# Performance work log

Measured on AMD Instinct MI355X. Metric: run time of the kernel, lower is better.

The kernel has to match this reference:

```python
import jax, jax.numpy as jnp
import numpy as np
import math

B, D, H, DK = 24, 64, 8, 8
N, M, CN = 256, 64, 16
VW, VC, CE, WE = 30000, 128, 200, 300

FREQS = jnp.asarray(np.array([10000.0 ** (-i / D) if i % 2 == 0 else -(10000.0 ** (-(i - 1) / D)) for i in range(D)], dtype=np.float32)[:, None])
PHASES = jnp.asarray(np.array([0.0 if i % 2 == 0 else math.pi / 2 for i in range(D)], dtype=np.float32)[:, None])

def _norm(x, eps=1e-6):
    mu = x.mean(-1, keepdims=True)
    var = ((x - mu) ** 2).sum(-1, keepdims=True) / (x.shape[-1] - 1)  # torch std is unbiased
    return (x - mu) / (jnp.sqrt(var) + eps)

def _pos_enc(x):
    pos = jnp.arange(x.shape[-1], dtype=x.dtype)[None, :]
    return jnp.sin(jnp.sin(pos * FREQS + PHASES)) + x  # double sin kept faithful to source

def _conv1d(x, w, groups=1, pad=0, b=None):
    y = jax.lax.conv_general_dilated(x, w, (1,), [(pad, pad)], dimension_numbers=('NCH', 'OIH', 'NCH'), feature_group_count=groups)
    return y if b is None else y + b[None, :, None]

def _dwsep1d(x, dw, pw, db=None, pb=None):
    y = _conv1d(x, dw, groups=x.shape[1], pad=dw.shape[-1] // 2, b=db)
    return _conv1d(y, pw, b=pb)

def _conv2d(x, w, groups=1, pad=0, b=None):
    y = jax.lax.conv_general_dilated(x, w, (1, 1), [(pad, pad), (pad, pad)], dimension_numbers=('NCHW', 'OIHW', 'NCHW'), feature_group_count=groups)
    return y if b is None else y + b[None, :, None, None]

def _highway(x, lw, lb, gw, gb):
    x = x.transpose(0, 2, 1)  # [B,L,D]
    for i in range(lw.shape[0]):
        g = jax.nn.sigmoid(jnp.einsum('bld,od->blo', x, gw[i]) + gb[i])
        nl = jax.nn.relu(jnp.einsum('bld,od->blo', x, lw[i]) + lb[i])
        x = g * nl + (1.0 - g) * x
    return x.transpose(0, 2, 1)

def _embed(ch, wd, e2dw, e2db, e2pw, e2pb, e1dw, e1db, e1pw, e1pb, hlw, hlb, hgw, hgb):
    ch = ch.transpose(0, 3, 1, 2)  # [B,CE,L,CN]
    ch = _conv2d(ch, e2dw, groups=CE, pad=2, b=e2db)
    ch = _conv2d(ch, e2pw, b=e2pb)
    ch = jax.nn.relu(ch).max(axis=3)  # [B,D,L]
    wd = wd.transpose(0, 2, 1)  # [B,WE,L]
    emb = jnp.concatenate([ch, wd], axis=1)
    emb = _dwsep1d(emb, e1dw, e1pw, e1db, e1pb)
    return _highway(emb, hlw, hlb, hgw, hgb)

def _self_att(x, wq, wk, wv, wo):
    Qh = jnp.einsum('hbkd,bdl->hbkl', wq, x)
    Kh = jnp.einsum('hbkd,bdl->hbkl', wk, x)
    Vh = jnp.einsum('hbkd,bdl->hbkl', wv, x)
    scores = jnp.einsum('hbkl,hbkm->hblm', Qh, Kh) / math.sqrt(DK)
    att = jax.nn.softmax(scores, axis=2)  # torch softmax dim=1 over [B,l,m]
    head = jnp.einsum('hbvl,hblm->hbvm', Vh, att)
    head = head.transpose(1, 0, 2, 3).reshape(B, H * DK, x.shape[-1])
    return jnp.einsum('bod,bdl->bol', wo, head)

def _enc_block(x, dw, pw, wq, wk, wv, wo, W):
    out = _pos_enc(x)
    res = out
    for i in range(dw.shape[0]):
        out = jax.nn.relu(_dwsep1d(_norm(out), dw[i], pw[i]))
        out = res + out
        res = out  # dropout is a no-op in this deterministic reference
    out = res + _self_att(_norm(out), wq, wk, wv, wo)
    res = out
    out = jax.nn.relu(jnp.einsum('bod,bdl->bol', W, _norm(out)))
    return res + out

def _cq_att(C, Q, W):
    # S[b,i,j] = W . [Q[:,j]; C[:,i]; Q[:,j]*C[:,i]] -- vectorized trilinear similarity
    wq, wc, wm = W[:, 0, :D], W[:, 0, D:2 * D], W[:, 0, 2 * D:]
    S = (jnp.einsum('bd,bdn->bn', wc, C)[:, :, None]
         + jnp.einsum('bd,bdm->bm', wq, Q)[:, None, :]
         + jnp.einsum('bdn,bdm->bnm', C * wm[:, :, None], Q))
    S1 = jax.nn.softmax(S, axis=2)
    S2 = jax.nn.softmax(S, axis=1)
    A = jnp.einsum('bdm,bnm->bdn', Q, S1)
    X = jnp.einsum('bnm,bkm->bnk', S1, S2)  # S1 @ S2^T
    Bm = jnp.einsum('bdn,bkn->bdk', C, X)   # C @ X^T
    return jnp.concatenate([C, A, C * A, C * Bm], axis=1)

def _pointer(M0, M1, M2, w0, w1):
    Y0 = jnp.einsum('bd,bdn->bn', w0[:, 0], jnp.concatenate([M0, M1], axis=1))
    Y1 = jnp.einsum('bd,bdn->bn', w1[:, 0], jnp.concatenate([M0, M2], axis=1))
    return jax.nn.softmax(Y0, axis=1), jax.nn.softmax(Y1, axis=1)  # exp(log_softmax)

def _qanet(flt, Cwid, Ccid, Qwid, Qcid):
    (word_table, char_table,
     e2dw, e2db, e2pw, e2pb, e1dw, e1db, e1pw, e1pb,
     hlw, hlb, hgw, hgb,
     ce_dw, ce_pw, ce_wq, ce_wk, ce_wv, ce_wo, ce_w,
     qe_dw, qe_pw, qe_wq, qe_wk, qe_wv, qe_wo, qe_w,
     m0_dw, m0_pw, m0_wq, m0_wk, m0_wv, m0_wo, m0_w,
     m1_dw, m1_pw, m1_wq, m1_wk, m1_wv, m1_wo, m1_w,
     m2_dw, m2_pw, m2_wq, m2_wk, m2_wv, m2_wo, m2_w,
     cq_w, rs_dw, rs_pw, p_w0, p_w1) = flt
    emb_p = (e2dw, e2db, e2pw, e2pb, e1dw, e1db, e1pw, e1pb, hlw, hlb, hgw, hgb)
    C = _embed(char_table[Ccid], word_table[Cwid], *emb_p)
    Q = _embed(char_table[Qcid], word_table[Qwid], *emb_p)
    C = _enc_block(C, ce_dw, ce_pw, ce_wq, ce_wk, ce_wv, ce_wo, ce_w)
    Q = _enc_block(Q, qe_dw, qe_pw, qe_wq, qe_wk, qe_wv, qe_wo, qe_w)
    X = _cq_att(C, Q, cq_w)
    X = _dwsep1d(X, rs_dw, rs_pw)
    M0 = X
    for _ in range(7):
        M0 = _enc_block(M0, m0_dw, m0_pw, m0_wq, m0_wk, m0_wv, m0_wo, m0_w)
    M1 = M0
    for _ in range(7):
        M1 = _enc_block(M1, m1_dw, m1_pw, m1_wq, m1_wk, m1_wv, m1_wo, m1_w)
    M2 = M1
    for _ in range(7):
        M2 = _enc_block(M2, m2_dw, m2_pw, m2_wq, m2_wk, m2_wv, m2_wo, m2_w)
    return _pointer(M0, M1, M2, p_w0, p_w1)

def setup_inputs() -> dict:
    key = jax.random.key(0)
    ks = iter(jax.random.split(key, 80))
    rn = lambda shape, s=0.1: jax.random.normal(next(ks), shape, jnp.float32) * s
    inp = {}
    inp['word_table'] = rn((VW, WE), 1.0)
    inp['char_table'] = rn((VC, CE), 1.0)
    inp['e2dw'] = rn((CE, 1, 5, 5)); inp['e2db'] = jnp.zeros((CE,), jnp.float32)
    inp['e2pw'] = rn((D, CE, 1, 1)); inp['e2pb'] = jnp.zeros((D,), jnp.float32)
    inp['e1dw'] = rn((WE + D, 1, 5)); inp['e1db'] = jnp.zeros((WE + D,), jnp.float32)
    inp['e1pw'] = rn((D, WE + D, 1)); inp['e1pb'] = jnp.zeros((D,), jnp.float32)
    inp['hlw'] = rn((2, D, D)); inp['hlb'] = jnp.zeros((2, D), jnp.float32)
    inp['hgw'] = rn((2, D, D)); inp['hgb'] = jnp.zeros((2, D), jnp.float32)
    for p, (cnum, k_) in [('ce', (4, 7)), ('qe', (4, 7)), ('m0', (2, 5)), ('m1', (2, 5)), ('m2', (2, 5))]:
        inp[p + '_dw'] = rn((cnum, D, 1, k_))
        inp[p + '_pw'] = rn((cnum, D, D, 1))
        inp[p + '_wq'] = rn((H, B, DK, D))
        inp[p + '_wk'] = rn((H, B, DK, D))
        inp[p + '_wv'] = rn((H, B, DK, D))
        inp[p + '_wo'] = rn((B, D, D))
        inp[p + '_w'] = rn((B, D, D))
    inp['cq_w'] = rn((B, 1, 3 * D))
    inp['rs_dw'] = rn((4 * D, 1, 5))
    inp['rs_pw'] = rn((D, 4 * D, 1))
    inp['p_w0'] = rn((B, 1, 2 * D))
    inp['p_w1'] = rn((B, 1, 2 * D))
    inp['Cwid'] = jax.random.randint(next(ks), (B, N), 0, VW)
    inp['Ccid'] = jax.random.randint(next(ks), (B, N, CN), 0, VC)
    inp['Qwid'] = jax.random.randint(next(ks), (B, M), 0, VW)
    inp['Qcid'] = jax.random.randint(next(ks), (B, M, CN), 0, VC)
    return inp

def reference(word_table, char_table, e2dw, e2db, e2pw, e2pb, e1dw, e1db, e1pw, e1pb, hlw, hlb, hgw, hgb, ce_dw, ce_pw, ce_wq, ce_wk, ce_wv, ce_wo, ce_w, qe_dw, qe_pw, qe_wq, qe_wk, qe_wv, qe_wo, qe_w, m0_dw, m0_pw, m0_wq, m0_wk, m0_wv, m0_wo, m0_w, m1_dw, m1_pw, m1_wq, m1_wk, m1_wv, m1_wo, m1_w, m2_dw, m2_pw, m2_wq, m2_wk, m2_wv, m2_wo, m2_w, cq_w, rs_dw, rs_pw, p_w0, p_w1, Cwid, Ccid, Qwid, Qcid):
    flt = (word_table, char_table, e2dw, e2db, e2pw, e2pb, e1dw, e1db, e1pw, e1pb, hlw, hlb, hgw, hgb, ce_dw, ce_pw, ce_wq, ce_wk, ce_wv, ce_wo, ce_w, qe_dw, qe_pw, qe_wq, qe_wk, qe_wv, qe_wo, qe_w, m0_dw, m0_pw, m0_wq, m0_wk, m0_wv, m0_wo, m0_w, m1_dw, m1_pw, m1_wq, m1_wk, m1_wv, m1_wo, m1_w, m2_dw, m2_pw, m2_wq, m2_wk, m2_wv, m2_wo, m2_w, cq_w, rs_dw, rs_pw, p_w0, p_w1)
    p0, p1 = _qanet(flt, Cwid, Ccid, Qwid, Qcid)
    return p0, p1
```

## Files before the change

kernel.cpp:

```cpp
#include <hip/hip_runtime.h>
#include <math.h>

constexpr int B = 24, HH = 8;
constexpr int NN = 256, MQ = 64;
constexpr int EC = 364;

#define PI_2 1.5707963267948966f

__device__ __forceinline__ void combine_stats(const float* __restrict__ parts,
                                              int row, int NT, float Lf,
                                              float& mu, float& inv) {
  float s = 0.f, q = 0.f;
  for (int t = 0; t < NT; ++t) {
    s += parts[((size_t)row * 4 + t) * 2];
    q += parts[((size_t)row * 4 + t) * 2 + 1];
  }
  mu = s / Lf;
  float var = (q - s * mu) / (Lf - 1.f);
  if (var < 0.f) var = 0.f;
  inv = 1.f / (sqrtf(var) + 1e-6f);
}

__global__ void k_prep(float* __restrict__ tab,
                       const float* __restrict__ e2pw, const float* __restrict__ e1pw,
                       const float* __restrict__ hlw, const float* __restrict__ hgw,
                       const float* __restrict__ e2dw,
                       float* __restrict__ pwT, float* __restrict__ e1pwT,
                       float* __restrict__ hlwT, float* __restrict__ hgwT,
                       float* __restrict__ dwT) {
  int blk = blockIdx.x;
  if (blk < 64) {
    int d = blk, l = threadIdx.x;
    float fr = ((d & 1) == 0) ? powf(10000.f, -(float)d / 64.f)
                              : -powf(10000.f, -(float)(d - 1) / 64.f);
    float ph = (d & 1) ? PI_2 : 0.f;
    tab[d * 256 + l] = sinf(sinf((float)l * fr + ph));
    return;
  }
  int i = (blk - 64) * 256 + threadIdx.x;
  if (i < 12800) {
    int ce = i >> 6, o = i & 63;
    pwT[i] = e2pw[o * 200 + ce];
    return;
  }
  i -= 12800;
  if (i < 23296) {
    int c = i >> 6, o = i & 63;
    e1pwT[i] = e1pw[o * EC + c];
    return;
  }
  i -= 23296;
  if (i < 8192) {
    int layer = i >> 12, rem = i & 4095;
    int d = rem >> 6, o = rem & 63;
    hlwT[i] = hlw[layer * 4096 + o * 64 + d];
    return;
  }
  i -= 8192;
  if (i < 8192) {
    int layer = i >> 12, rem = i & 4095;
    int d = rem >> 6, o = rem & 63;
    hgwT[i] = hgw[layer * 4096 + o * 64 + d];
    return;
  }
  i -= 8192;
  if (i < 5000) {
    int t = i / 200, ce = i % 200;
    dwT[i] = e2dw[ce * 25 + t];
  }
}

__global__ void k_posadd_stats(float* __restrict__ XC, float* __restrict__ XQ,
                               const float* __restrict__ tab,
                               float* __restrict__ partsC, float* __restrict__ partsQ) {
  int which = blockIdx.y;
  float* X = which ? XQ : XC;
  float* parts = which ? partsQ : partsC;
  int L = which ? 64 : 256;
  int row = blockIdx.x * 4 + (threadIdx.x >> 6);
  int lane = threadIdx.x & 63;
  int d = row & 63;
  float* xr = X + (size_t)row * L;
  int NT = L >> 6;
  for (int t = 0; t < NT; ++t) {
    int l = t * 64 + lane;
    float v = xr[l] + tab[d * 256 + l];
    xr[l] = v;
    float s = v, q = v * v;
#pragma unroll
    for (int o = 32; o > 0; o >>= 1) { s += __shfl_xor(s, o); q += __shfl_xor(q, o); }
    if (lane == 0) {
      parts[((size_t)row * 4 + t) * 2] = s;
      parts[((size_t)row * 4 + t) * 2 + 1] = q;
    }
  }
}

template<int K>
__global__ __launch_bounds__(1024) void k_fconv(
    const float* __restrict__ XiC, float* __restrict__ XoC,
    const float* __restrict__ XiQ, float* __restrict__ XoQ,
    const float* __restrict__ dwC, const float* __restrict__ pwC,
    const float* __restrict__ dwQ, const float* __restrict__ pwQ,
    const float* __restrict__ pinC, float* __restrict__ poutC,
    const float* __restrict__ pinQ, float* __restrict__ poutQ) {
  constexpr int H = K / 2, SW = 64 + 2 * H;
  __shared__ float smu[64], sinv[64];
  __shared__ float sN[64 * SW];
  __shared__ float sD[64 * 65];
  __shared__ __align__(16) float sWt[4096];
  int b = blockIdx.x, t = blockIdx.y;
  const float *Xin, *dw, *pw, *pin; float *Xout, *pout; int L, tile;
  if (t < 4) { Xin = XiC; Xout = XoC; dw = dwC; pw = pwC; pin = pinC; pout = poutC; L = 256; tile = t; }
  else       { Xin = XiQ; Xout = XoQ; dw = dwQ; pw = pwQ; pin = pinQ; pout = poutQ; L = 64;  tile = 0; }
  int lt = tile * 64;
  int tid = threadIdx.x;
  int NT = L >> 6;
  if (tid < 64) combine_stats(pin, b * 64 + tid, NT, (float)L, smu[tid], sinv[tid]);
  for (int i = tid; i < 1024; i += 1024)
    ((float4*)sWt)[i] = ((const float4*)pw)[i];
  const float* Xb = Xin + (size_t)b * 64 * L;
  int l = tid & 63, og = tid >> 6;
  float rres[4];
#pragma unroll
  for (int j = 0; j < 4; ++j)
    rres[j] = Xb[(size_t)(og * 4 + j) * L + lt + l];
  __syncthreads();
  for (int i = tid; i < 64 * SW; i += 1024) {
    int c = i / SW, jj = i % SW;
    int gl = lt + jj - H;
    sN[i] = (gl >= 0 && gl < L) ? (Xb[(size_t)c * L + gl] - smu[c]) * sinv[c] : 0.f;
  }
  __syncthreads();
  for (int i = tid; i < 4096; i += 1024) {
    int c = i >> 6, ll = i & 63;
    float acc = 0.f;
#pragma unroll
    for (int k = 0; k < K; ++k) acc += sN[c * SW + ll + k] * dw[c * K + k];
    sD[c * 65 + ll] = acc;
  }
  __syncthreads();
  float acc[4];
#pragma unroll
  for (int j = 0; j < 4; ++j) acc[j] = 0.f;
  for (int c = 0; c < 64; ++c) {
    float av = sD[c * 65 + l];
#pragma unroll
    for (int j = 0; j < 4; ++j) acc[j] += sWt[(og * 4 + j) * 64 + c] * av;
  }
  __syncthreads();
  float* Ob = Xout + (size_t)b * 64 * L;
#pragma unroll
  for (int j = 0; j < 4; ++j) {
    int o = og * 4 + j;
    float v = rres[j] + fmaxf(acc[j], 0.f);
    Ob[(size_t)o * L + lt + l] = v;
    sD[o * 65 + l] = v;
  }
  __syncthreads();
  if (tid < 64) {
    int o = tid;
    float s = 0.f, q = 0.f;
    for (int l2 = 0; l2 < 64; ++l2) { float v = sD[o * 65 + l2]; s += v; q += v * v; }
    pout[((size_t)(b * 64 + o) * 4 + tile) * 2] = s;
    pout[((size_t)(b * 64 + o) * 4 + tile) * 2 + 1] = q;
  }
}

template<bool NORM, bool RELU, bool STATS, bool ADDTAB, bool DUAL>
__global__ __launch_bounds__(1024) void k_matmul2(
    const float* __restrict__ AC, const float* __restrict__ WC,
    const float* __restrict__ resC, float* __restrict__ outC2,
    const float* __restrict__ pinC, float* __restrict__ poutC,
    const float* __restrict__ AQ, const float* __restrict__ WQ,
    const float* __restrict__ resQ, float* __restrict__ outQ2,
    const float* __restrict__ pinQ, float* __restrict__ poutQ,
    float* __restrict__ outNextC, const float* __restrict__ tab) {
  __shared__ float sA[64 * 65];
  __shared__ __align__(16) float sW[4096];
  __shared__ float smu[64], sinv[64];
  int b = blockIdx.x, t = blockIdx.y;
  const float *A, *W, *res, *pin; float *outp, *pout; int L, tile;
  if (t < 4) { A = AC; W = WC; res = resC; outp = outC2; pin = pinC; pout = poutC; L = 256; tile = t; }
  else       { A = AQ; W = WQ; res = resQ; outp = outQ2; pin = pinQ; pout = poutQ; L = 64;  tile = 0; }
  int lt = tile * 64;
  int tid = threadIdx.x;
  int NT = L >> 6;
  if (NORM && tid < 64) combine_stats(pin, b * 64 + tid, NT, (float)L, smu[tid], sinv[tid]);
  const float* Wb = W + (size_t)b * 4096;
  for (int i = tid; i < 1024; i += 1024)
    ((float4*)sW)[i] = ((const float4*)Wb)[i];
  int l = tid & 63, og = tid >> 6;
  float rres[4], rtab[4];
#pragma unroll
  for (int j = 0; j < 4; ++j) {
    int o = og * 4 + j;
    rres[j] = res[((size_t)b * 64 + o) * L + lt + l];
    if (ADDTAB || DUAL) rtab[j] = tab[o * 256 + lt + l];
  }
  if (NORM) __syncthreads();
  const float* Ab = A + (size_t)b * 64 * L;
  for (int i = tid; i < 1024; i += 1024) {
    int c = i >> 4, lq = (i & 15) * 4;
    float4 v = *(const float4*)(Ab + (size_t)c * L + lt + lq);
    if (NORM) {
      float mu = smu[c], iv = sinv[c];
      v.x = (v.x - mu) * iv; v.y = (v.y - mu) * iv;
      v.z = (v.z - mu) * iv; v.w = (v.w - mu) * iv;
    }
    sA[c * 65 + lq] = v.x; sA[c * 65 + lq + 1] = v.y;
    sA[c * 65 + lq + 2] = v.z; sA[c * 65 + lq + 3] = v.w;
  }
  __syncthreads();
  float acc[4];
#pragma unroll
  for (int j = 0; j < 4; ++j) acc[j] = 0.f;
  for (int c = 0; c < 64; ++c) {
    float av = sA[c * 65 + l];
#pragma unroll
    for (int j = 0; j < 4; ++j) acc[j] += sW[(og * 4 + j) * 64 + c] * av;
  }
  if (STATS) __syncthreads();
#pragma unroll
  for (int j = 0; j < 4; ++j) {
    int o = og * 4 + j;
    float v = acc[j];
    if (RELU) v = fmaxf(v, 0.f);
    v += rres[j];
    if (DUAL) {
      float vn = v + rtab[j];
      outp[((size_t)b * 64 + o) * L + lt + l] = v;
      outNextC[((size_t)b * 64 + o) * L + lt + l] = vn;
      if (STATS) sA[o * 65 + l] = vn;
    } else {
      if (ADDTAB) v += rtab[j];
      outp[((size_t)b * 64 + o) * L + lt + l] = v;
      if (STATS) sA[o * 65 + l] = v;
    }
  }
  if (STATS) {
    __syncthreads();
    if (tid < 64) {
      int o = tid;
      float s = 0.f, q = 0.f;
      for (int l2 = 0; l2 < 64; ++l2) { float v = sA[o * 65 + l2]; s += v; q += v * v; }
      pout[((size_t)(b * 64 + o) * 4 + tile) * 2] = s;
      pout[((size_t)(b * 64 + o) * 4 + tile) * 2 + 1] = q;
    }
  }
}

__global__ __launch_bounds__(256) void k_resize(
    const float* __restrict__ Xcat, const float* __restrict__ dw,
    const float* __restrict__ pw, const float* __restrict__ tab,
    float* __restrict__ out, float* __restrict__ parts) {
  __shared__ float sA[64 * 65];
  int b = blockIdx.x, lt = blockIdx.y * 64;
  int l = threadIdx.x & 63, og = threadIdx.x >> 6;
  float acc[16];
#pragma unroll
  for (int j = 0; j < 16; ++j) acc[j] = 0.f;
  for (int c0 = 0; c0 < 256; c0 += 64) {
    __syncthreads();
    for (int i = threadIdx.x; i < 4096; i += 256) {
      int c = (i >> 6) + c0, ll = (i & 63) + lt;
      const float* xr = Xcat + ((size_t)b * 256 + c) * 256;
      float a = 0.f;
#pragma unroll
      for (int k = 0; k < 5; ++k) {
        int p = ll + k - 2;
        if (p >= 0 && p < 256) a += xr[p] * dw[c * 5 + k];
      }
      sA[(i >> 6) * 65 + (i & 63)] = a;
    }
    __syncthreads();
    for (int c = 0; c < 64; ++c) {
      float av = sA[c * 65 + l];
#pragma unroll
      for (int j = 0; j < 16; ++j)
        acc[j] += pw[(size_t)(og * 16 + j) * 256 + c0 + c] * av;
    }
  }
  __syncthreads();
#pragma unroll
  for (int j = 0; j < 16; ++j) {
    int o = og * 16 + j;
    float v = acc[j] + tab[o * 256 + lt + l];
    out[((size_t)b * 64 + o) * 256 + lt + l] = v;
    sA[o * 65 + l] = v;
  }
  __syncthreads();
  if (threadIdx.x < 64) {
    int o = threadIdx.x;
    float s = 0.f, q = 0.f;
    for (int l2 = 0; l2 < 64; ++l2) { float v = sA[o * 65 + l2]; s += v; q += v * v; }
    parts[((size_t)(b * 64 + o) * 4 + blockIdx.y) * 2] = s;
    parts[((size_t)(b * 64 + o) * 4 + blockIdx.y) * 2 + 1] = q;
  }
}

__global__ __launch_bounds__(1024) void k_att(
    const float* __restrict__ XC, const float* __restrict__ partsC,
    const float* __restrict__ wqC, const float* __restrict__ wkC,
    const float* __restrict__ wvC, float* __restrict__ hcC,
    const float* __restrict__ XQ, const float* __restrict__ partsQ,
    const float* __restrict__ wqQ, const float* __restrict__ wkQ,
    const float* __restrict__ wvQ, float* __restrict__ hcQ) {
  int h = blockIdx.x, b2 = blockIdx.y;
  const float *X, *parts, *wq, *wk, *wv; float* hc; int L, b;
  if (b2 < B) { X = XC; parts = partsC; wq = wqC; wk = wkC; wv = wvC; hc = hcC; L = 256; b = b2; }
  else        { X = XQ; parts = partsQ; wq = wqQ; wk = wkQ; wv = wvQ; hc = hcQ; L = 64;  b = b2 - B; }
  __shared__ float smu[64], sinv[64];
  __shared__ float sX[64 * 65];
  __shared__ float sQ[2048], sK8[2048], sV[2048];
  __shared__ float swq[512], swk[512], swv[512];
  __shared__ float pmx[1024], psum[1024];
  int tid = threadIdx.x;
  int NT = L >> 6;
  if (tid < 64) combine_stats(parts, b * 64 + tid, NT, (float)L, smu[tid], sinv[tid]);
  size_t woff = (size_t)(h * B + b) * 512;
  if (tid < 512) {
    swq[tid] = wq[woff + tid];
    swk[tid] = wk[woff + tid];
    swv[tid] = wv[woff + tid];
  }
  __syncthreads();
  const float* Xb = X + (size_t)b * 64 * L;
  for (int lt = 0; lt < L; lt += 64) {
    for (int i = tid; i < 4096; i += 1024) {
      int d = i >> 6, l = i & 63;
      sX[d * 65 + l] = (Xb[(size_t)d * L + lt + l] - smu[d]) * sinv[d];
    }
    __syncthreads();
    if (tid < 512) {
      int k = tid >> 6, l = tid & 63;
      float aq = 0.f, ak = 0.f, av = 0.f;
      for (int d = 0; d < 64; ++d) {
        float x = sX[d * 65 + l];
        aq += swq[k * 64 + d] * x;
        ak += swk[k * 64 + d] * x;
        av += swv[k * 64 + d] * x;
      }
      sQ[k * L + lt + l] = aq; sK8[k * L + lt + l] = ak; sV[k * L + lt + l] = av;
    }
    __syncthreads();
  }
  const float scale = 0.35355339059327373f;
  int m = tid & 255, qt = tid >> 8;
  int L4 = L >> 2;
  float mx = -1e30f, sum = 0.f, acc[8];
#pragma unroll
  for (int v = 0; v < 8; ++v) acc[v] = 0.f;
  if (m < L) {
    float kc[8];
#pragma unroll
    for (int k = 0; k < 8; ++k) kc[k] = sK8[k * L + m];
    int l0 = qt * L4, l1 = l0 + L4;
    for (int l = l0; l < l1; ++l) {
      float s = 0.f;
#pragma unroll
      for (int k = 0; k < 8; ++k) s += sQ[k * L + l] * kc[k];
      s *= scale;
      if (s <= mx) {
        float p = __expf(s - mx);
        sum += p;
#pragma unroll
        for (int v = 0; v < 8; ++v) acc[v] += p * sV[v * L + l];
      } else {
        float corr = __expf(mx - s);
        sum = sum * corr + 1.f;
#pragma unroll
        for (int v = 0; v < 8; ++v) acc[v] = acc[v] * corr + sV[v * L + l];
// ... 349 lines not shown
  out[sel * 6144 + b * 256 + n] = e / s;
}

extern "C" void kernel_launch(void* const* d_in, const int* in_sizes, int n_in,
                              void* d_out, int out_size, void* d_ws, size_t ws_size,
                              hipStream_t stream) {
  const float* word_table = (const float*)d_in[0];
  const float* char_table = (const float*)d_in[1];
  const float* e2dw = (const float*)d_in[2];
  const float* e2db = (const float*)d_in[3];
  const float* e2pw = (const float*)d_in[4];
  const float* e2pb = (const float*)d_in[5];
  const float* e1dw = (const float*)d_in[6];
  const float* e1db = (const float*)d_in[7];
  const float* e1pw = (const float*)d_in[8];
  const float* e1pb = (const float*)d_in[9];
  const float* hlw = (const float*)d_in[10];
  const float* hlb = (const float*)d_in[11];
  const float* hgw = (const float*)d_in[12];
  const float* hgb = (const float*)d_in[13];
  const float *enc_dw[5], *enc_pw[5], *enc_wq[5], *enc_wk[5], *enc_wv[5], *enc_wo[5], *enc_w[5];
  for (int p = 0; p < 5; ++p) {
    enc_dw[p] = (const float*)d_in[14 + 7 * p + 0];
    enc_pw[p] = (const float*)d_in[14 + 7 * p + 1];
    enc_wq[p] = (const float*)d_in[14 + 7 * p + 2];
    enc_wk[p] = (const float*)d_in[14 + 7 * p + 3];
    enc_wv[p] = (const float*)d_in[14 + 7 * p + 4];
    enc_wo[p] = (const float*)d_in[14 + 7 * p + 5];
    enc_w[p]  = (const float*)d_in[14 + 7 * p + 6];
  }
  const float* cq_w  = (const float*)d_in[49];
  const float* rs_dw = (const float*)d_in[50];
  const float* rs_pw = (const float*)d_in[51];
  const float* p_w0  = (const float*)d_in[52];
  const float* p_w1  = (const float*)d_in[53];
  const int* Cwid = (const int*)d_in[54];
  const int* Ccid = (const int*)d_in[55];
  const int* Qwid = (const int*)d_in[56];
  const int* Qcid = (const int*)d_in[57];
  float* out = (float*)d_out;

  float* ws = (float*)d_ws;
  float* postab = ws;
  float* U    = ws + 16384;
  float* Xcat = ws + 409600;
  float* CX   = ws + 1982464;
  float* Sb   = ws + 2375680;
  float* QX   = ws + 2768896;
  float* CS2  = ws + 2867200;
  float* rmax = ws + 2965504;
  float* rsum = ws + 2971648;
  float* cmax = ws + 2977792;
  float* csum = ws + 2979328;
  float* P0   = ws + 2980864;
  float* P1   = ws + 2993152;
  float* pwT  = ws + 3005440;
  float* e1pwT= ws + 3018240;
  float* hlwT = ws + 3041536;
  float* hgwT = ws + 3049728;
  float* dwT  = ws + 3057920;
  float* P0Q  = ws + 3062920;
  float* P1Q  = ws + 3075208;
  float* UQ   = ws + 3087496;
  float* M0 = CX; float* M1 = Sb; float* M2 = Xcat;
  float* E1C = Xcat;
  float* E1Q = Xcat + 393216;
  (void)out_size; (void)in_sizes; (void)n_in; (void)ws_size;

  auto run_enc = [&](float* X, float* Xnext, int p) {
    for (int rep = 0; rep < 7; ++rep) {
      float* pin = P0; float* pout = P1;
      float* Xi = X; float* Xo = U;
      for (int i = 0; i < 2; ++i) {
        hipLaunchKernelGGL((k_fconv<5>), dim3(B, 4), dim3(1024), 0, stream,
                           (const float*)Xi, Xo, (const float*)nullptr, (float*)nullptr,
                           enc_dw[p] + i * 64 * 5, enc_pw[p] + (size_t)i * 4096,
                           (const float*)nullptr, (const float*)nullptr,
                           pin, pout, (const float*)nullptr, (float*)nullptr);
        { float* t = pin; pin = pout; pout = t; }
        { float* t = Xi; Xi = Xo; Xo = t; }
      }
      k_att<<<dim3(HH, B), 1024, 0, stream>>>(X, pin, enc_wq[p], enc_wk[p], enc_wv[p], U,
                                              (const float*)nullptr, (const float*)nullptr,
                                              (const float*)nullptr, (const float*)nullptr,
                                              (const float*)nullptr, (float*)nullptr);
      hipLaunchKernelGGL((k_matmul2<false, false, true, false, false>), dim3(B, 4), dim3(1024), 0, stream,
                         (const float*)U, enc_wo[p], (const float*)X, X, (const float*)nullptr, pout,
                         (const float*)nullptr, (const float*)nullptr, (const float*)nullptr,
                         (float*)nullptr, (const float*)nullptr, (float*)nullptr,
                         (float*)nullptr, (const float*)nullptr);
      if (rep < 6)
        hipLaunchKernelGGL((k_matmul2<true, true, true, true, false>), dim3(B, 4), dim3(1024), 0, stream,
                           (const float*)X, enc_w[p], (const float*)X, X, pout, P0,
                           (const float*)nullptr, (const float*)nullptr, (const float*)nullptr,
                           (float*)nullptr, (const float*)nullptr, (float*)nullptr,
                           (float*)nullptr, (const float*)postab);
      else if (Xnext)
        hipLaunchKernelGGL((k_matmul2<true, true, true, false, true>), dim3(B, 4), dim3(1024), 0, stream,
                           (const float*)X, enc_w[p], (const float*)X, X, pout, P0,
                           (const float*)nullptr, (const float*)nullptr, (const float*)nullptr,
                           (float*)nullptr, (const float*)nullptr, (float*)nullptr,
                           Xnext, (const float*)postab);
      else
        hipLaunchKernelGGL((k_matmul2<true, true, false, false, false>), dim3(B, 4), dim3(1024), 0, stream,
                           (const float*)X, enc_w[p], (const float*)X, X, pout, (float*)nullptr,
                           (const float*)nullptr, (const float*)nullptr, (const float*)nullptr,
                           (float*)nullptr, (const float*)nullptr, (float*)nullptr,
                           (float*)nullptr, (const float*)nullptr);
    }
  };

  k_prep<<<289, 256, 0, stream>>>(postab, e2pw, e1pw, hlw, hgw, e2dw,
                                  pwT, e1pwT, hlwT, hgwT, dwT);
  k_charembed<<<dim3(NN + MQ, B), 256, 0, stream>>>(Ccid, Qcid, char_table, dwT, e2db, pwT, e2pb, E1C, E1Q);
  k_embhw<<<dim3(NN + MQ, B), 64, 0, stream>>>(E1C, E1Q, Cwid, Qwid, word_table, e1dw, e1db,
                                               e1pwT, e1pb, hlwT, hlb, hgwT, hgb, CX, QX);
  {
    k_posadd_stats<<<dim3(384, 2), 256, 0, stream>>>(CX, QX, postab, P0, P0Q);
    float *pinC = P0, *poutC = P1, *pinQ = P0Q, *poutQ = P1Q;
    float *XiC = CX, *XoC = U, *XiQ = QX, *XoQ = UQ;
    for (int i = 0; i < 4; ++i) {
      hipLaunchKernelGGL((k_fconv<7>), dim3(B, 5), dim3(1024), 0, stream,
                         (const float*)XiC, XoC, (const float*)XiQ, XoQ,
                         enc_dw[0] + i * 64 * 7, enc_pw[0] + (size_t)i * 4096,
                         enc_dw[1] + i * 64 * 7, enc_pw[1] + (size_t)i * 4096,
                         pinC, poutC, pinQ, poutQ);
      { float* t = pinC; pinC = poutC; poutC = t; }
      { float* t = pinQ; pinQ = poutQ; poutQ = t; }
      { float* t = XiC; XiC = XoC; XoC = t; }
      { float* t = XiQ; XiQ = XoQ; XoQ = t; }
    }
    k_att<<<dim3(HH, 2 * B), 1024, 0, stream>>>(CX, pinC, enc_wq[0], enc_wk[0], enc_wv[0], U,
                                                QX, pinQ, enc_wq[1], enc_wk[1], enc_wv[1], UQ);
    hipLaunchKernelGGL((k_matmul2<false, false, true, false, false>), dim3(B, 5), dim3(1024), 0, stream,
                       (const float*)U, enc_wo[0], (const float*)CX, CX, (const float*)nullptr, poutC,
                       (const float*)UQ, enc_wo[1], (const float*)QX, QX, (const float*)nullptr, poutQ,
                       (float*)nullptr, (const float*)nullptr);
    hipLaunchKernelGGL((k_matmul2<true, true, false, false, false>), dim3(B, 5), dim3(1024), 0, stream,
                       (const float*)CX, enc_w[0], (const float*)CX, CX, poutC, (float*)nullptr,
                       (const float*)QX, enc_w[1], (const float*)QX, QX, poutQ, (float*)nullptr,
                       (float*)nullptr, (const float*)nullptr);
  }
  k_cqS<<<dim3(B, 4), 256, 0, stream>>>(CX, QX, cq_w, Sb, rmax, rsum);
  k_cqcol<<<B, 64, 0, stream>>>(Sb, cmax, csum);
  k_cqA_CS2<<<dim3(B, 5), 256, 0, stream>>>(CX, QX, Sb, rmax, rsum, cmax, csum, Xcat, CS2);
  k_cqBm<<<dim3(B, 4), 256, 0, stream>>>(CX, CS2, Sb, rmax, rsum, Xcat);
  k_resize<<<dim3(B, 4), 256, 0, stream>>>(Xcat, rs_dw, rs_pw, postab, M0, P0);
  run_enc(M0, M1, 2);
  run_enc(M1, M2, 3);
  run_enc(M2, nullptr, 4);
  k_pointer2<<<dim3(B, 2), 256, 0, stream>>>(M0, M1, M2, p_w0, p_w1, out);
}
```

Baseline: 1.999 ms.

## Fuse encoder conv pairs and wo/FFN into per-batch whole-sequence kernels

```diff
diff --git a/kernel.cpp b/kernel.cpp
--- a/kernel.cpp
+++ b/kernel.cpp
@@ -6,19 +6,29 @@
 constexpr int EC = 364;
 
 #define PI_2 1.5707963267948966f
-
-__device__ __forceinline__ void combine_stats(const float* __restrict__ parts,
-                                              int row, int NT, float Lf,
-                                              float& mu, float& inv) {
+#define CONV_LDS (36992 * 4)
+#define SMALL_LDS (18560 * 4)
+
+__device__ __forceinline__ void block_stats(const float* __restrict__ sX,
+                                            float* __restrict__ scratch,
+                                            float* __restrict__ smu,
+                                            float* __restrict__ sinv,
+                                            int L, int tid) {
+  int row = tid >> 4, sub = tid & 15;
   float s = 0.f, q = 0.f;
-  for (int t = 0; t < NT; ++t) {
-    s += parts[((size_t)row * 4 + t) * 2];
-    q += parts[((size_t)row * 4 + t) * 2 + 1];
-  }
-  mu = s / Lf;
-  float var = (q - s * mu) / (Lf - 1.f);
-  if (var < 0.f) var = 0.f;
-  inv = 1.f / (sqrtf(var) + 1e-6f);
+  for (int l2 = sub; l2 < L; l2 += 16) { float v = sX[row * L + l2]; s += v; q += v * v; }
+  scratch[row * 16 + sub] = s;
+  scratch[1024 + row * 16 + sub] = q;
+  __syncthreads();
+  if (tid < 64) {
+    float ss = 0.f, qq = 0.f;
+    for (int k = 0; k < 16; ++k) { ss += scratch[tid * 16 + k]; qq += scratch[1024 + tid * 16 + k]; }
+    float mu = ss / (float)L;
+    float var = (qq - ss * mu) / ((float)L - 1.f);
+    if (var < 0.f) var = 0.f;
+    smu[tid] = mu; sinv[tid] = 1.f / (sqrtf(var) + 1e-6f);
+  }
+  __syncthreads();
 }
 
 __global__ void k_prep(float* __restrict__ tab,
@@ -38,17 +48,9 @@
     return;
   }
   int i = (blk - 64) * 256 + threadIdx.x;
-  if (i < 12800) {
-    int ce = i >> 6, o = i & 63;
-    pwT[i] = e2pw[o * 200 + ce];
-    return;
-  }
+  if (i < 12800) { int ce = i >> 6, o = i & 63; pwT[i] = e2pw[o * 200 + ce]; return; }
   i -= 12800;
-  if (i < 23296) {
-    int c = i >> 6, o = i & 63;
-    e1pwT[i] = e1pw[o * EC + c];
-    return;
-  }
+  if (i < 23296) { int c = i >> 6, o = i & 63; e1pwT[i] = e1pw[o * EC + c]; return; }
   i -= 23296;
   if (i < 8192) {
     int layer = i >> 12, rem = i & 4095;
@@ -64,206 +66,194 @@
     return;
   }
   i -= 8192;
-  if (i < 5000) {
-    int t = i / 200, ce = i % 200;
-    dwT[i] = e2dw[ce * 25 + t];
-  }
-}
-
-__global__ void k_posadd_stats(float* __restrict__ XC, float* __restrict__ XQ,
-                               const float* __restrict__ tab,
-                               float* __restrict__ partsC, float* __restrict__ partsQ) {
-  int which = blockIdx.y;
-  float* X = which ? XQ : XC;
-  float* parts = which ? partsQ : partsC;
-  int L = which ? 64 : 256;
-  int row = blockIdx.x * 4 + (threadIdx.x >> 6);
-  int lane = threadIdx.x & 63;
-  int d = row & 63;
-  float* xr = X + (size_t)row * L;
-  int NT = L >> 6;
-  for (int t = 0; t < NT; ++t) {
-    int l = t * 64 + lane;
-    float v = xr[l] + tab[d * 256 + l];
-    xr[l] = v;
-    float s = v, q = v * v;
-#pragma unroll
-    for (int o = 32; o > 0; o >>= 1) { s += __shfl_xor(s, o); q += __shfl_xor(q, o); }
-    if (lane == 0) {
-      parts[((size_t)row * 4 + t) * 2] = s;
-      parts[((size_t)row * 4 + t) * 2 + 1] = q;
-    }
-  }
+  if (i < 5000) { int t = i / 200, ce = i % 200; dwT[i] = e2dw[ce * 25 + t]; }
+}
+
+__global__ __launch_bounds__(1024) void k_posadd(float* __restrict__ XC, float* __restrict__ XQ,
+                                                 const float* __restrict__ tab,
+                                                 float* __restrict__ SMc, float* __restrict__ SIc,
+                                                 float* __restrict__ SMq, float* __restrict__ SIq) {
+  extern __shared__ float sm[];
+  float* sX = sm; float* scratch = sm + 16384; float* smu = sm + 18432; float* sinv = sm + 18496;
+  int b = blockIdx.x, side = blockIdx.y;
+  float* X = side ? XQ : XC;
+  int L = side ? 64 : 256;
+  float* SM = side ? SMq : SMc;
+  float* SI = side ? SIq : SIc;
+  int tid = threadIdx.x;
+  float* Xb = X + (size_t)b * 64 * L;
+  for (int i = tid; i < 64 * L; i += 1024) {
+    int d = i / L, l = i % L;
+    float v = Xb[i] + tab[d * 256 + l];
+    Xb[i] = v; sX[i] = v;
+  }
+  __syncthreads();
+  block_stats(sX, scratch, smu, sinv, L, tid);
+  if (tid < 64) { SM[b * 64 + tid] = smu[tid]; SI[b * 64 + tid] = sinv[tid]; }
+}
+
+template<int K, int L>
+__device__ void conv2_impl(float* __restrict__ sm, float* __restrict__ X,
+                           const float* __restrict__ dw, const float* __restrict__ pw,
+                           float* __restrict__ SM, float* __restrict__ SI, int b, int nconv) {
+  constexpr int PER = (64 * L) / 1024;
+  float* sX = sm; float* sD = sm + 16384; float* sW = sm + 32768;
+  float* smu = sm + 36864; float* sinv = sm + 36928;
+  int tid = threadIdx.x;
+  int l = tid % L, og = tid / L;
+  float* Xb = X + (size_t)b * 64 * L;
+  for (int i = tid; i < 64 * L; i += 1024) sX[i] = Xb[i];
+  if (tid < 64) { smu[tid] = SM[b * 64 + tid]; sinv[tid] = SI[b * 64 + tid]; }
+  __syncthreads();
+  for (int cv = 0; cv < nconv; ++cv) {
+    {
+      const float* pwc = pw + cv * 4096;
+      for (int i = tid; i < 1024; i += 1024)
+        ((float4*)sW)[i] = ((const float4*)pwc)[i];
+    }
+    for (int i = tid; i < 64 * L; i += 1024) {
+      int c = i / L, ll = i % L;
+      float mu = smu[c], iv = sinv[c];
+      float acc = 0.f;
+#pragma unroll
+      for (int k = 0; k < K; ++k) {
+        int p = ll + k - K / 2;
+        float x = (p >= 0 && p < L) ? (sX[c * L + p] - mu) * iv : 0.f;
+        acc += x * dw[cv * 64 * K + c * K + k];
+      }
+      sD[i] = acc;
+    }
+    __syncthreads();
+    float acc[PER];
+#pragma unroll
+    for (int j = 0; j < PER; ++j) acc[j] = 0.f;
+    for (int c = 0; c < 64; ++c) {
+      float av = sD[c * L + l];
+#pragma unroll
+      for (int j = 0; j < PER; ++j) acc[j] += sW[(og * PER + j) * 64 + c] * av;
+    }
+#pragma unroll
+    for (int j = 0; j < PER; ++j) {
+      int o = og * PER + j;
+      sX[o * L + l] = sX[o * L + l] + fmaxf(acc[j], 0.f);
+    }
+    __syncthreads();
+    block_stats(sX, sD, smu, sinv, L, tid);
+  }
+  for (int i = tid; i < 64 * L; i += 1024) Xb[i] = sX[i];
+  if (tid < 64) { SM[b * 64 + tid] = smu[tid]; SI[b * 64 + tid] = sinv[tid]; }
 }
 
 template<int K>
-__global__ __launch_bounds__(1024) void k_fconv(
-    const float* __restrict__ XiC, float* __restrict__ XoC,
-    const float* __restrict__ XiQ, float* __restrict__ XoQ,
-    const float* __restrict__ dwC, const float* __restrict__ pwC,
-    const float* __restrict__ dwQ, const float* __restrict__ pwQ,
-    const float* __restrict__ pinC, float* __restrict__ poutC,
-    const float* __restrict__ pinQ, float* __restrict__ poutQ) {
-  constexpr int H = K / 2, SW = 64 + 2 * H;
-  __shared__ float smu[64], sinv[64];
-  __shared__ float sN[64 * SW];
-  __shared__ float sD[64 * 65];
-  __shared__ __align__(16) float sWt[4096];
-  int b = blockIdx.x, t = blockIdx.y;
-  const float *Xin, *dw, *pw, *pin; float *Xout, *pout; int L, tile;
-  if (t < 4) { Xin = XiC; Xout = XoC; dw = dwC; pw = pwC; pin = pinC; pout = poutC; L = 256; tile = t; }
-  else       { Xin = XiQ; Xout = XoQ; dw = dwQ; pw = pwQ; pin = pinQ; pout = poutQ; L = 64;  tile = 0; }
-  int lt = tile * 64;
+__global__ __launch_bounds__(1024) void k_conv2(
+    float* XC, float* XQ,
+    const float* dwC, const float* pwC, const float* dwQ, const float* pwQ,
+    float* SMc, float* SIc, float* SMq, float* SIq, int nconv) {
+  extern __shared__ float sm[];
+  int b = blockIdx.x;
+  if (blockIdx.y == 0) conv2_impl<K, 256>(sm, XC, dwC, pwC, SMc, SIc, b, nconv);
+  else                 conv2_impl<K, 64>(sm, XQ, dwQ, pwQ, SMq, SIq, b, nconv);
+}
+
+template<int L>
+__device__ void woff_impl(float* __restrict__ sm, const float* __restrict__ U,
+                          float* __restrict__ X, const float* __restrict__ wo,
+                          const float* __restrict__ w, float* __restrict__ SM,
+                          float* __restrict__ SI, float* __restrict__ Xnext,
+                          const float* __restrict__ tab, int b, int mode) {
+  constexpr int PER = (64 * L) / 1024;
+  float* sX = sm; float* sD = sm + 16384; float* sW = sm + 32768;
+  float* smu = sm + 36864; float* sinv = sm + 36928;
   int tid = threadIdx.x;
-  int NT = L >> 6;
-  if (tid < 64) combine_stats(pin, b * 64 + tid, NT, (float)L, smu[tid], sinv[tid]);
-  for (int i = tid; i < 1024; i += 1024)
-    ((float4*)sWt)[i] = ((const float4*)pw)[i];
-  const float* Xb = Xin + (size_t)b * 64 * L;
-  int l = tid & 63, og = tid >> 6;
-  float rres[4];
-#pragma unroll
-  for (int j = 0; j < 4; ++j)
-    rres[j] = Xb[(size_t)(og * 4 + j) * L + lt + l];
-  __syncthreads();
-  for (int i = tid; i < 64 * SW; i += 1024) {
-    int c = i / SW, jj = i % SW;
-    int gl = lt + jj - H;
-    sN[i] = (gl >= 0 && gl < L) ? (Xb[(size_t)c * L + gl] - smu[c]) * sinv[c] : 0.f;
-  }
-  __syncthreads();
-  for (int i = tid; i < 4096; i += 1024) {
-    int c = i >> 6, ll = i & 63;
-    float acc = 0.f;
-#pragma unroll
-    for (int k = 0; k < K; ++k) acc += sN[c * SW + ll + k] * dw[c * K + k];
-    sD[c * 65 + ll] = acc;
-  }
-  __syncthreads();
-  float acc[4];
-#pragma unroll
-  for (int j = 0; j < 4; ++j) acc[j] = 0.f;
+  int l = tid % L, og = tid / L;
+  const float* Ub = U + (size_t)b * 64 * L;
+  float* Xb = X + (size_t)b * 64 * L;
+  for (int i = tid; i < 64 * L; i += 1024) { sX[i] = Ub[i]; sD[i] = Xb[i]; }
+  {
+    const float* Wb = wo + (size_t)b * 4096;
+    for (int i = tid; i < 1024; i += 1024)
+      ((float4*)sW)[i] = ((const float4*)Wb)[i];
+  }
+  __syncthreads();
+  float acc[PER];
+#pragma unroll
+  for (int j = 0; j < PER; ++j) acc[j] = 0.f;
   for (int c = 0; c < 64; ++c) {
-    float av = sD[c * 65 + l];
-#pragma unroll
-    for (int j = 0; j < 4; ++j) acc[j] += sWt[(og * 4 + j) * 64 + c] * av;
-  }
-  __syncthreads();
-  float* Ob = Xout + (size_t)b * 64 * L;
-#pragma unroll
-  for (int j = 0; j < 4; ++j) {
-    int o = og * 4 + j;
-    float v = rres[j] + fmaxf(acc[j], 0.f);
-    Ob[(size_t)o * L + lt + l] = v;
-    sD[o * 65 + l] = v;
-  }
-  __syncthreads();
-  if (tid < 64) {
-    int o = tid;
-    float s = 0.f, q = 0.f;
-    for (int l2 = 0; l2 < 64; ++l2) { float v = sD[o * 65 + l2]; s += v; q += v * v; }
-    pout[((size_t)(b * 64 + o) * 4 + tile) * 2] = s;
-    pout[((size_t)(b * 64 + o) * 4 + tile) * 2 + 1] = q;
-  }
-}
-
-template<bool NORM, bool RELU, bool STATS, bool ADDTAB, bool DUAL>
-__global__ __launch_bounds__(1024) void k_matmul2(
-    const float* __restrict__ AC, const float* __restrict__ WC,
-    const float* __restrict__ resC, float* __restrict__ outC2,
-    const float* __restrict__ pinC, float* __restrict__ poutC,
-    const float* __restrict__ AQ, const float* __restrict__ WQ,
-    const float* __restrict__ resQ, float* __restrict__ outQ2,
-    const float* __restrict__ pinQ, float* __restrict__ poutQ,
-    float* __restrict__ outNextC, const float* __restrict__ tab) {
-  __shared__ float sA[64 * 65];
-  __shared__ __align__(16) float sW[4096];
-  __shared__ float smu[64], sinv[64];
-  int b = blockIdx.x, t = blockIdx.y;
-  const float *A, *W, *res, *pin; float *outp, *pout; int L, tile;
-  if (t < 4) { A = AC; W = WC; res = resC; outp = outC2; pin = pinC; pout = poutC; L = 256; tile = t; }
-  else       { A = AQ; W = WQ; res = resQ; outp = outQ2; pin = pinQ; pout = poutQ; L = 64;  tile = 0; }
-  int lt = tile * 64;
-  int tid = threadIdx.x;
-  int NT = L >> 6;
-  if (NORM && tid < 64) combine_stats(pin, b * 64 + tid, NT, (float)L, smu[tid], sinv[tid]);
-  const float* Wb = W + (size_t)b * 4096;
-  for (int i = tid; i < 1024; i += 1024)
-    ((float4*)sW)[i] = ((const float4*)Wb)[i];
-  int l = tid & 63, og = tid >> 6;
-  float rres[4], rtab[4];
-#pragma unroll
-  for (int j = 0; j < 4; ++j) {
-    int o = og * 4 + j;
-    rres[j] = res[((size_t)b * 64 + o) * L + lt + l];
-    if (ADDTAB || DUAL) rtab[j] = tab[o * 256 + lt + l];
-  }
-  if (NORM) __syncthreads();
-  const float* Ab = A + (size_t)b * 64 * L;
-  for (int i = tid; i < 1024; i += 1024) {
-    int c = i >> 4, lq = (i & 15) * 4;
-    float4 v = *(const float4*)(Ab + (size_t)c * L + lt + lq);
-    if (NORM) {
-      float mu = smu[c], iv = sinv[c];
-      v.x = (v.x - mu) * iv; v.y = (v.y - mu) * iv;
-      v.z = (v.z - mu) * iv; v.w = (v.w - mu) * iv;
-    }
-    sA[c * 65 + lq] = v.x; sA[c * 65 + lq + 1] = v.y;
-    sA[c * 65 + lq + 2] = v.z; sA[c * 65 + lq + 3] = v.w;
-  }
-  __syncthreads();
-  float acc[4];
-#pragma unroll
-  for (int j = 0; j < 4; ++j) acc[j] = 0.f;
+    float av = sX[c * L + l];
+#pragma unroll
+    for (int j = 0; j < PER; ++j) acc[j] += sW[(og * PER + j) * 64 + c] * av;
+  }
+  __syncthreads();
+#pragma unroll
+  for (int j = 0; j < PER; ++j) {
+    int o = og * PER + j;
+    sX[o * L + l] = sD[o * L + l] + acc[j];
+  }
+  __syncthreads();
+  block_stats(sX, sD, smu, sinv, L, tid);
+  {
+    const float* Wb = w + (size_t)b * 4096;
+    for (int i = tid; i < 1024; i += 1024)
+      ((float4*)sW)[i] = ((const float4*)Wb)[i];
+  }
+  __syncthreads();
+#pragma unroll
+  for (int j = 0; j < PER; ++j) acc[j] = 0.f;
   for (int c = 0; c < 64; ++c) {
-    float av = sA[c * 65 + l];
-#pragma unroll
-    for (int j = 0; j < 4; ++j) acc[j] += sW[(og * 4 + j) * 64 + c] * av;
-  }
-  if (STATS) __syncthreads();
-#pragma unroll
-  for (int j = 0; j < 4; ++j) {
-    int o = og * 4 + j;
-    float v = acc[j];
-    if (RELU) v = fmaxf(v, 0.f);
-    v += rres[j];
-    if (DUAL) {
-      float vn = v + rtab[j];
-      outp[((size_t)b * 64 + o) * L + lt + l] = v;
-      outNextC[((size_t)b * 64 + o) * L + lt + l] = vn;
-      if (STATS) sA[o * 65 + l] = vn;
+    float av = (sX[c * L + l] - smu[c]) * sinv[c];
+#pragma unroll
+    for (int j = 0; j < PER; ++j) acc[j] += sW[(og * PER + j) * 64 + c] * av;
+  }
+  __syncthreads();
+#pragma unroll
+  for (int j = 0; j < PER; ++j) {
+    int o = og * PER + j;
+    float v = sX[o * L + l] + fmaxf(acc[j], 0.f);
+    if (mode == 0) {
+      float vn = v + tab[o * 256 + l];
+      Xb[o * L + l] = vn; sX[o * L + l] = vn;
+    } else if (mode == 1) {
+      float vn = v + tab[o * 256 + l];
+      Xb[o * L + l] = v;
+      Xnext[(size_t)b * 64 * L + o * L + l] = vn;
+      sX[o * L + l] = vn;
     } else {
-      if (ADDTAB) v += rtab[j];
-      outp[((size_t)b * 64 + o) * L + lt + l] = v;
-      if (STATS) sA[o * 65 + l] = v;
-    }
-  }
-  if (STATS) {
-    __syncthreads();
-    if (tid < 64) {
-      int o = tid;
-      float s = 0.f, q = 0.f;
-      for (int l2 = 0; l2 < 64; ++l2) { float v = sA[o * 65 + l2]; s += v; q += v * v; }
-      pout[((size_t)(b * 64 + o) * 4 + tile) * 2] = s;
-      pout[((size_t)(b * 64 + o) * 4 + tile) * 2 + 1] = q;
-    }
-  }
-}
-
-__global__ __launch_bounds__(256) void k_resize(
+      Xb[o * L + l] = v;
+    }
+  }
+  if (mode < 2) {
+    __syncthreads();
+    block_stats(sX, sD, smu, sinv, L, tid);
+    if (tid < 64) { SM[b * 64 + tid] = smu[tid]; SI[b * 64 + tid] = sinv[tid]; }
+  }
+}
+
+__global__ __launch_bounds__(1024) void k_woff(
+    const float* UC, const float* UQ, float* XC, float* XQ,
+    const float* woC, const float* woQ, const float* wC, const float* wQ,
+    float* SMc, float* SIc, float* SMq, float* SIq,
+    float* Xnext, const float* tab, int mode) {
+  extern __shared__ float sm[];
+  int b = blockIdx.x;
+  if (blockIdx.y == 0) woff_impl<256>(sm, UC, XC, woC, wC, SMc, SIc, Xnext, tab, b, mode);
+  else                 woff_impl<64>(sm, UQ, XQ, woQ, wQ, SMq, SIq, nullptr, tab, b, mode);
+}
+
+__global__ __launch_bounds__(1024) void k_resize(
     const float* __restrict__ Xcat, const float* __restrict__ dw,
     const float* __restrict__ pw, const float* __restrict__ tab,
-    float* __restrict__ out, float* __restrict__ parts) {
-  __shared__ float sA[64 * 65];
-  int b = blockIdx.x, lt = blockIdx.y * 64;
-  int l = threadIdx.x & 63, og = threadIdx.x >> 6;
+    float* __restrict__ out, float* __restrict__ SM, float* __restrict__ SI) {
+  extern __shared__ float sm[];
+  float* sA = sm; float* scratch = sm + 16384; float* smu = sm + 18432; float* sinv = sm + 18496;
+  int b = blockIdx.x, tid = threadIdx.x;
+  int l = tid & 255, og = tid >> 8;
   float acc[16];
 #pragma unroll
   for (int j = 0; j < 16; ++j) acc[j] = 0.f;
   for (int c0 = 0; c0 < 256; c0 += 64) {
     __syncthreads();
-    for (int i = threadIdx.x; i < 4096; i += 256) {
-      int c = (i >> 6) + c0, ll = (i & 63) + lt;
+    for (int i = tid; i < 16384; i += 1024) {
+      int c = (i >> 8) + c0, ll = i & 255;
       const float* xr = Xcat + ((size_t)b * 256 + c) * 256;
       float a = 0.f;
 #pragma unroll
@@ -271,11 +261,11 @@
         int p = ll + k - 2;
         if (p >= 0 && p < 256) a += xr[p] * dw[c * 5 + k];
       }
-      sA[(i >> 6) * 65 + (i & 63)] = a;
+      sA[i] = a;
     }
     __syncthreads();
     for (int c = 0; c < 64; ++c) {
-      float av = sA[c * 65 + l];
+      float av = sA[c * 256 + l];
 #pragma unroll
       for (int j = 0; j < 16; ++j)
         acc[j] += pw[(size_t)(og * 16 + j) * 256 + c0 + c] * av;
@@ -285,39 +275,33 @@
 #pragma unroll
   for (int j = 0; j < 16; ++j) {
     int o = og * 16 + j;
-    float v = acc[j] + tab[o * 256 + lt + l];
-    out[((size_t)b * 64 + o) * 256 + lt + l] = v;
-    sA[o * 65 + l] = v;
-  }
-  __syncthreads();
-  if (threadIdx.x < 64) {
-    int o = threadIdx.x;
-    float s = 0.f, q = 0.f;
-    for (int l2 = 0; l2 < 64; ++l2) { float v = sA[o * 65 + l2]; s += v; q += v * v; }
-    parts[((size_t)(b * 64 + o) * 4 + blockIdx.y) * 2] = s;
-    parts[((size_t)(b * 64 + o) * 4 + blockIdx.y) * 2 + 1] = q;
-  }
+    float v = acc[j] + tab[o * 256 + l];
+    out[((size_t)b * 64 + o) * 256 + l] = v;
+    sA[o * 256 + l] = v;
+  }
+  __syncthreads();
+  block_stats(sA, scratch, smu, sinv, 256, tid);
+  if (tid < 64) { SM[b * 64 + tid] = smu[tid]; SI[b * 64 + tid] = sinv[tid]; }
 }
 
 __global__ __launch_bounds__(1024) void k_att(
-    const float* __restrict__ XC, const float* __restrict__ partsC,
+    const float* __restrict__ XC, const float* __restrict__ SMc, const float* __restrict__ SIc,
     const float* __restrict__ wqC, const float* __restrict__ wkC,
     const float* __restrict__ wvC, float* __restrict__ hcC,
-    const float* __restrict__ XQ, const float* __restrict__ partsQ,
+    const float* __restrict__ XQ, const float* __restrict__ SMq, const float* __restrict__ SIq,
     const float* __restrict__ wqQ, const float* __restrict__ wkQ,
     const float* __restrict__ wvQ, float* __restrict__ hcQ) {
   int h = blockIdx.x, b2 = blockIdx.y;
-  const float *X, *parts, *wq, *wk, *wv; float* hc; int L, b;
-  if (b2 < B) { X = XC; parts = partsC; wq = wqC; wk = wkC; wv = wvC; hc = hcC; L = 256; b = b2; }
-  else        { X = XQ; parts = partsQ; wq = wqQ; wk = wkQ; wv = wvQ; hc = hcQ; L = 64;  b = b2 - B; }
+  const float *X, *SM, *SI, *wq, *wk, *wv; float* hc; int L, b;
+  if (b2 < B) { X = XC; SM = SMc; SI = SIc; wq = wqC; wk = wkC; wv = wvC; hc = hcC; L = 256; b = b2; }
+  else        { X = XQ; SM = SMq; SI = SIq; wq = wqQ; wk = wkQ; wv = wvQ; hc = hcQ; L = 64;  b = b2 - B; }
   __shared__ float smu[64], sinv[64];
   __shared__ float sX[64 * 65];
   __shared__ float sQ[2048], sK8[2048], sV[2048];
   __shared__ float swq[512], swk[512], swv[512];
   __shared__ float pmx[1024], psum[1024];
   int tid = threadIdx.x;
-  int NT = L >> 6;
-  if (tid < 64) combine_stats(parts, b * 64 + tid, NT, (float)L, smu[tid], sinv[tid]);
+  if (tid < 64) { smu[tid] = SM[b * 64 + tid]; sinv[tid] = SI[b * 64 + tid]; }
   size_t woff = (size_t)(h * B + b) * 512;
   if (tid < 512) {
     swq[tid] = wq[woff + tid];
@@ -773,15 +757,15 @@
   float* rsum = ws + 2971648;
   float* cmax = ws + 2977792;
   float* csum = ws + 2979328;
-  float* P0   = ws + 2980864;
-  float* P1   = ws + 2993152;
+  float* SMC  = ws + 2980864;
+  float* SIC  = ws + 2982400;
+  float* SMQ  = ws + 2983936;
+  float* SIQ  = ws + 2985472;
   float* pwT  = ws + 3005440;
   float* e1pwT= ws + 3018240;
   float* hlwT = ws + 3041536;
   float* hgwT = ws + 3049728;
   float* dwT  = ws + 3057920;
-  float* P0Q  = ws + 3062920;
-  float* P1Q  = ws + 3075208;
   float* UQ   = ws + 3087496;
   float* M0 = CX; float* M1 = Sb; float* M2 = Xcat;
   float* E1C = Xcat;
@@ -790,44 +774,21 @@
 
   auto run_enc = [&](float* X, float* Xnext, int p) {
     for (int rep = 0; rep < 7; ++rep) {
-      float* pin = P0; float* pout = P1;
-      float* Xi = X; float* Xo = U;
-      for (int i = 0; i < 2; ++i) {
-        hipLaunchKernelGGL((k_fconv<5>), dim3(B, 4), dim3(1024), 0, stream,
-                           (const float*)Xi, Xo, (const float*)nullptr, (float*)nullptr,
-                           enc_dw[p] + i * 64 * 5, enc_pw[p] + (size_t)i * 4096,
-                           (const float*)nullptr, (const float*)nullptr,
-                           pin, pout, (const float*)nullptr, (float*)nullptr);
-        { float* t = pin; pin = pout; pout = t; }
-        { float* t = Xi; Xi = Xo; Xo = t; }
-      }
-      k_att<<<dim3(HH, B), 1024, 0, stream>>>(X, pin, enc_wq[p], enc_wk[p], enc_wv[p], U,
+      hipLaunchKernelGGL((k_conv2<5>), dim3(B, 1), dim3(1024), CONV_LDS, stream,
+                         X, (float*)nullptr, enc_dw[p], enc_pw[p],
+                         (const float*)nullptr, (const float*)nullptr,
+                         SMC, SIC, (float*)nullptr, (float*)nullptr, 2);
+      k_att<<<dim3(HH, B), 1024, 0, stream>>>(X, SMC, SIC, enc_wq[p], enc_wk[p], enc_wv[p], U,
                                               (const float*)nullptr, (const float*)nullptr,
                                               (const float*)nullptr, (const float*)nullptr,
-                                              (const float*)nullptr, (float*)nullptr);
-      hipLaunchKernelGGL((k_matmul2<false, false, true, false, false>), dim3(B, 4), dim3(1024), 0, stream,
-                         (const float*)U, enc_wo[p], (const float*)X, X, (const float*)nullptr, pout,
-                         (const float*)nullptr, (const float*)nullptr, (const float*)nullptr,
-                         (float*)nullptr, (const float*)nullptr, (float*)nullptr,
-                         (float*)nullptr, (const float*)nullptr);
-      if (rep < 6)
-        hipLaunchKernelGGL((k_matmul2<true, true, true, true, false>), dim3(B, 4), dim3(1024), 0, stream,
-                           (const float*)X, enc_w[p], (const float*)X, X, pout, P0,
-                           (const float*)nullptr, (const float*)nullptr, (const float*)nullptr,
-                           (float*)nullptr, (const float*)nullptr, (float*)nullptr,
-                           (float*)nullptr, (const float*)postab);
-      else if (Xnext)
-        hipLaunchKernelGGL((k_matmul2<true, true, true, false, true>), dim3(B, 4), dim3(1024), 0, stream,
-                           (const float*)X, enc_w[p], (const float*)X, X, pout, P0,
-                           (const float*)nullptr, (const float*)nullptr, (const float*)nullptr,
-                           (float*)nullptr, (const float*)nullptr, (float*)nullptr,
-                           Xnext, (const float*)postab);
-      else
-        hipLaunchKernelGGL((k_matmul2<true, true, false, false, false>), dim3(B, 4), dim3(1024), 0, stream,
-                           (const float*)X, enc_w[p], (const float*)X, X, pout, (float*)nullptr,
-                           (const float*)nullptr, (const float*)nullptr, (const float*)nullptr,
-                           (float*)nullptr, (const float*)nullptr, (float*)nullptr,
-                           (float*)nullptr, (const float*)nullptr);
+                                              (const float*)nullptr, (const float*)nullptr,
+                                              (float*)nullptr);
+      int mode = (rep < 6) ? 0 : (Xnext ? 1 : 2);
+      hipLaunchKernelGGL(k_woff, dim3(B, 1), dim3(1024), CONV_LDS, stream,
+                         (const float*)U, (const float*)nullptr, X, (float*)nullptr,
+                         enc_wo[p], (const float*)nullptr, enc_w[p], (const float*)nullptr,
+                         SMC, SIC, (float*)nullptr, (float*)nullptr,
+                         Xnext, (const float*)postab, mode);
     }
   };
 
@@ -837,36 +798,29 @@
   k_embhw<<<dim3(NN + MQ, B), 64, 0, stream>>>(E1C, E1Q, Cwid, Qwid, word_table, e1dw, e1db,
                                                e1pwT, e1pb, hlwT, hlb, hgwT, hgb, CX, QX);
   {
-    k_posadd_stats<<<dim3(384, 2), 256, 0, stream>>>(CX, QX, postab, P0, P0Q);
-    float *pinC = P0, *poutC = P1, *pinQ = P0Q, *poutQ = P1Q;
-    float *XiC = CX, *XoC = U, *XiQ = QX, *XoQ = UQ;
-    for (int i = 0; i < 4; ++i) {
-      hipLaunchKernelGGL((k_fconv<7>), dim3(B, 5), dim3(1024), 0, stream,
-                         (const float*)XiC, XoC, (const float*)XiQ, XoQ,
-                         enc_dw[0] + i * 64 * 7, enc_pw[0] + (size_t)i * 4096,
-                         enc_dw[1] + i * 64 * 7, enc_pw[1] + (size_t)i * 4096,
-                         pinC, poutC, pinQ, poutQ);
-      { float* t = pinC; pinC = poutC; poutC = t; }
-      { float* t = pinQ; pinQ = poutQ; poutQ = t; }
-      { float* t = XiC; XiC = XoC; XoC = t; }
-      { float* t = XiQ; XiQ = XoQ; XoQ = t; }
-    }
-    k_att<<<dim3(HH, 2 * B), 1024, 0, stream>>>(CX, pinC, enc_wq[0], enc_wk[0], enc_wv[0], U,
-                                                QX, pinQ, enc_wq[1], enc_wk[1], enc_wv[1], UQ);
-    hipLaunchKernelGGL((k_matmul2<false, false, true, false, false>), dim3(B, 5), dim3(1024), 0, stream,
-                       (const float*)U, enc_wo[0], (const float*)CX, CX, (const float*)nullptr, poutC,
-                       (const float*)UQ, enc_wo[1], (const float*)QX, QX, (const float*)nullptr, poutQ,
-                       (float*)nullptr, (const float*)nullptr);
-    hipLaunchKernelGGL((k_matmul2<true, true, false, false, false>), dim3(B, 5), dim3(1024), 0, stream,
-                       (const float*)CX, enc_w[0], (const float*)CX, CX, poutC, (float*)nullptr,
-                       (const float*)QX, enc_w[1], (const float*)QX, QX, poutQ, (float*)nullptr,
-                       (float*)nullptr, (const float*)nullptr);
+    hipLaunchKernelGGL(k_posadd, dim3(B, 2), dim3(1024), SMALL_LDS, stream,
+                       CX, QX, (const float*)postab, SMC, SIC, SMQ, SIQ);
+    hipLaunchKernelGGL((k_conv2<7>), dim3(B, 2), dim3(1024), CONV_LDS, stream,
+                       CX, QX, enc_dw[0], enc_pw[0], enc_dw[1], enc_pw[1],
+                       SMC, SIC, SMQ, SIQ, 2);
+    hipLaunchKernelGGL((k_conv2<7>), dim3(B, 2), dim3(1024), CONV_LDS, stream,
+                       CX, QX, enc_dw[0] + 2 * 64 * 7, enc_pw[0] + 2 * 4096,
+                       enc_dw[1] + 2 * 64 * 7, enc_pw[1] + 2 * 4096,
+                       SMC, SIC, SMQ, SIQ, 2);
+    k_att<<<dim3(HH, 2 * B), 1024, 0, stream>>>(CX, SMC, SIC, enc_wq[0], enc_wk[0], enc_wv[0], U,
+                                                QX, SMQ, SIQ, enc_wq[1], enc_wk[1], enc_wv[1], UQ);
+    hipLaunchKernelGGL(k_woff, dim3(B, 2), dim3(1024), CONV_LDS, stream,
+                       (const float*)U, (const float*)UQ, CX, QX,
+                       enc_wo[0], enc_wo[1], enc_w[0], enc_w[1],
+                       SMC, SIC, SMQ, SIQ,
+                       (float*)nullptr, (const float*)postab, 2);
   }
   k_cqS<<<dim3(B, 4), 256, 0, stream>>>(CX, QX, cq_w, Sb, rmax, rsum);
   k_cqcol<<<B, 64, 0, stream>>>(Sb, cmax, csum);
   k_cqA_CS2<<<dim3(B, 5), 256, 0, stream>>>(CX, QX, Sb, rmax, rsum, cmax, csum, Xcat, CS2);
   k_cqBm<<<dim3(B, 4), 256, 0, stream>>>(CX, CS2, Sb, rmax, rsum, Xcat);
-  k_resize<<<dim3(B, 4), 256, 0, stream>>>(Xcat, rs_dw, rs_pw, postab, M0, P0);
+  hipLaunchKernelGGL(k_resize, dim3(B), dim3(1024), SMALL_LDS, stream,
+                     (const float*)Xcat, rs_dw, rs_pw, (const float*)postab, M0, SMC, SIC);
   run_enc(M0, M1, 2);
   run_enc(M1, M2, 3);
   run_enc(M2, nullptr, 4);
```

After: 3.712 ms. 85.7% more time.
